# Performance work log

Hardware: AMD Instinct MI355X
Metric: run time of the kernel (lower is better)

## Reference

```python
import jax, jax.numpy as jnp
import numpy as np

SEQ, BATCH, DIM = 2048, 32, 1024


def setup_inputs() -> dict:
    key = jax.random.key(0)
    k1, k2, k3, k4, k5 = jax.random.split(key, 5)
    scale = 1.0 / np.sqrt(DIM)
    return {
        "decoder_hidden": jax.random.normal(k1, (BATCH, 1, DIM), dtype=jnp.float32),
        "encoder_out": jax.random.normal(k2, (SEQ, BATCH, DIM), dtype=jnp.float32),
        "W_enc": jax.random.normal(k3, (DIM, DIM), dtype=jnp.float32) * scale,
        "W_dec": jax.random.normal(k4, (DIM, DIM), dtype=jnp.float32) * scale,
        "V_att": jax.random.normal(k5, (1, DIM), dtype=jnp.float32) * scale,
    }


def reference(decoder_hidden, encoder_out, W_enc, W_dec, V_att):
    # encoder_out: (seq, batch, dim); decoder_hidden: (batch, 1, dim)
    # torch Linear: y = x @ W.T with W of shape (out, in)
    keys = jnp.einsum('sbd,ed->bse', encoder_out, W_enc)      # (batch, seq, dim)
    query = decoder_hidden @ W_dec.T                           # (batch, 1, dim)
    scores = jnp.tanh(keys + query)                            # (batch, seq, dim)
    logits = jnp.einsum('bsd,d->bs', scores, V_att[0])         # (batch, seq)
    alpha = jax.nn.softmax(logits, axis=1)[..., None]          # (batch, seq, 1)
    # context = alpha^T @ encoder_out_permuted -> (batch, 1, dim)
    context = jnp.einsum('bs,sbd->bd', alpha[..., 0], encoder_out)[:, None, :]
    return context, jnp.transpose(alpha, (2, 0, 1))            # (1, batch, seq)
```

## Files before the change

### kernel.cpp

```cpp
#include <hip/hip_runtime.h>
#include <hip/hip_bf16.h>
#include <math.h>

#define SEQ   2048
#define BATCH 32
#define DIM   1024
#define MROWS (SEQ*BATCH)
#define NT2   4
#define NCH   16
#define NKT   16

typedef __attribute__((ext_vector_type(8))) short short8;
typedef __attribute__((ext_vector_type(8))) unsigned short u16x8;
typedef __attribute__((ext_vector_type(4))) float f32x4;

__device__ __forceinline__ unsigned short f2bf(float f) {
  unsigned u = __builtin_bit_cast(unsigned, f);
  u += 0x7FFFu + ((u >> 16) & 1u);
  return (unsigned short)(u >> 16);
}

__device__ __forceinline__ void gl16(const unsigned short* g, unsigned short* l) {
  __builtin_amdgcn_global_load_lds(
      (const __attribute__((address_space(1))) unsigned int*)g,
      (__attribute__((address_space(3))) unsigned int*)l, 16, 0, 0);
}

__global__ __launch_bounds__(256) void conv_bf16_k(const float* __restrict__ src,
                                                   unsigned short* __restrict__ dst) {
  size_t i = ((size_t)blockIdx.x * 256 + threadIdx.x) * 8;
  f32x4 a = __builtin_nontemporal_load(reinterpret_cast<const f32x4*>(src + i));
  f32x4 b = __builtin_nontemporal_load(reinterpret_cast<const f32x4*>(src + i + 4));
  u16x8 o;
  o[0] = f2bf(a[0]); o[1] = f2bf(a[1]); o[2] = f2bf(a[2]); o[3] = f2bf(a[3]);
  o[4] = f2bf(b[0]); o[5] = f2bf(b[1]); o[6] = f2bf(b[2]); o[7] = f2bf(b[3]);
  *reinterpret_cast<u16x8*>(dst + i) = o;
}

__global__ __launch_bounds__(256) void qpart_k(const float* __restrict__ dh,
                                               const float* __restrict__ Wd,
                                               float* __restrict__ qpart) {
  const int bx = blockIdx.x;
  const int eb = bx & 3;
  const int dc = bx >> 2;
  __shared__ float ldh[BATCH][128];
  const int tid = threadIdx.x;
#pragma unroll
  for (int i = 0; i < 4; ++i) {
    int idx = tid + i * 256;
    int bb = idx >> 5, d4 = idx & 31;
    float4 v = *reinterpret_cast<const float4*>(&dh[(size_t)bb * DIM + dc * 128 + d4 * 4]);
    *reinterpret_cast<float4*>(&ldh[bb][d4 * 4]) = v;
  }
  __syncthreads();
  const int e = eb * 256 + tid;
  float acc[BATCH];
#pragma unroll
  for (int b = 0; b < BATCH; ++b) acc[b] = 0.f;
  for (int d4 = 0; d4 < 32; ++d4) {
    float4 w = *reinterpret_cast<const float4*>(&Wd[(size_t)e * DIM + dc * 128 + d4 * 4]);
#pragma unroll
    for (int b = 0; b < BATCH; ++b) {
      float4 h = *reinterpret_cast<const float4*>(&ldh[b][d4 * 4]);
      acc[b] += w.x * h.x + w.y * h.y + w.z * h.z + w.w * h.w;
    }
  }
#pragma unroll
  for (int b = 0; b < BATCH; ++b)
    qpart[((size_t)dc * BATCH + b) * DIM + e] = acc[b];
}

__global__ __launch_bounds__(256) void qred_k(const float* __restrict__ qpart,
                                              float* __restrict__ q) {
  int i = blockIdx.x * 256 + threadIdx.x;
  float s = 0.f;
#pragma unroll
  for (int dc = 0; dc < 8; ++dc) s += qpart[(size_t)dc * 32768 + i];
  q[i] = s;
}

#define BARR  __builtin_amdgcn_s_barrier()
#define VMC(n) asm volatile("s_waitcnt vmcnt(" #n ")" ::: "memory")

#define STAGE_A(t, h) do {                                                        \
    const unsigned short* gb_ = Abase + (size_t)(t) * 64;                         \
    char* lb_ = arena + (((t) & 1) * 65536) + (h) * 16384;                        \
    gl16(gb_ + (size_t)(gA0 + (h) * 64) * 1024 + cSt * 8,                         \
         (unsigned short*)lb_ + w * 512);                                         \
    gl16(gb_ + (size_t)(gA0 + 128 + (h) * 64) * 1024 + cSt * 8,                   \
         (unsigned short*)(lb_ + 8192) + w * 512);                                \
  } while (0)

#define STAGE_B(t, h) do {                                                        \
    const unsigned short* gb_ = Bbase + (size_t)(t) * 64;                         \
    char* lb_ = arena + (((t) & 1) * 65536) + 32768 + (h) * 16384;                \
    gl16(gb_ + (size_t)(gB0 + (h) * 32) * 1024 + cSt * 8,                         \
         (unsigned short*)lb_ + w * 512);                                         \
    gl16(gb_ + (size_t)(gB0 + 128 + (h) * 32) * 1024 + cSt * 8,                   \
         (unsigned short*)(lb_ + 8192) + w * 512);                                \
  } while (0)

#define LOAD_A(d, MH) do {                                                        \
    const char* bA_ = arena + (d) * 65536 + (MH) * 16384;                         \
    _Pragma("unroll") for (int i_ = 0; i_ < 4; ++i_)                              \
    _Pragma("unroll") for (int ks_ = 0; ks_ < 2; ++ks_) {                         \
      int lrow_ = wr * 64 + i_ * 16 + fr;                                         \
      int lc_ = (ks_ * 4 + kq) ^ (fr & 7);                                        \
      a[i_][ks_] = *(const short8*)(bA_ + lrow_ * 128 + lc_ * 16);                \
    } } while (0)

#define LOAD_B(d, NH) do {                                                        \
    const char* bB_ = arena + (d) * 65536 + 32768 + (NH) * 16384;                 \
    _Pragma("unroll") for (int j_ = 0; j_ < 2; ++j_)                              \
    _Pragma("unroll") for (int ks_ = 0; ks_ < 2; ++ks_) {                         \
      int lrow_ = wc * 32 + j_ * 16 + fr;                                         \
      int lc_ = (ks_ * 4 + kq) ^ (fr & 7);                                        \
      b[NH][j_][ks_] = *(const short8*)(bB_ + lrow_ * 128 + lc_ * 16);            \
    } } while (0)

#define DO_QUAD(MH, NH) do {                                                      \
    __builtin_amdgcn_s_setprio(1);                                                \
    _Pragma("unroll") for (int i_ = 0; i_ < 4; ++i_)                              \
    _Pragma("unroll") for (int j_ = 0; j_ < 2; ++j_)                              \
    _Pragma("unroll") for (int ks_ = 0; ks_ < 2; ++ks_)                           \
      acc[(MH) * 4 + i_][(NH) * 2 + j_] =                                         \
          __builtin_amdgcn_mfma_f32_16x16x32_bf16(                                \
              a[i_][ks_], b[NH][j_][ks_], acc[(MH) * 4 + i_][(NH) * 2 + j_],      \
              0, 0, 0);                                                           \
    __builtin_amdgcn_s_setprio(0);                                                \
  } while (0)

__global__ __launch_bounds__(512, 2) void gemm8p(const unsigned short* __restrict__ A,
                                                 const unsigned short* __restrict__ B,
                                                 const float* __restrict__ q,
                                                 const float* __restrict__ V,
                                                 float* __restrict__ lpart) {
  __shared__ __align__(16) char arena[131072];

  const int bid = blockIdx.x;
  const int wg = (bid & 7) * 128 + (bid >> 3);
  const int mt = wg >> 2, nt = wg & 3;
  const int row0 = mt * 256, col0 = nt * 256;
  const int tid = threadIdx.x;
  const int lane = tid & 63, w = tid >> 6;
  const int wr = w >> 2, wc = w & 3;
  const int fr = lane & 15, kq = lane >> 4;

  const int lr0 = tid >> 3;
  const int cSt = (tid & 7) ^ (lr0 & 7);
  const int gA0 = lr0;
  const int gB0 = (lr0 & 31) + (lr0 >> 5) * 64;

  const unsigned short* Abase = A + (size_t)row0 * DIM;
  const unsigned short* Bbase = B + (size_t)col0 * DIM;

  f32x4 acc[8][4];
#pragma unroll
  for (int i = 0; i < 8; ++i)
#pragma unroll
    for (int j = 0; j < 4; ++j) acc[i][j] = (f32x4)(0.f);

  short8 a[4][2];
  short8 b[2][2][2];

  STAGE_A(0, 0); STAGE_B(0, 0); STAGE_A(0, 1); STAGE_B(0, 1);
  STAGE_A(1, 0); STAGE_B(1, 0);
  VMC(0);
  BARR;

#pragma unroll 1
  for (int t2 = 0; t2 < NKT; t2 += 2) {
    const bool last = (t2 == NKT - 2);
    LOAD_A(0, 0); LOAD_B(0, 0);
    STAGE_A(t2 + 1, 1);
    BARR; DO_QUAD(0, 0); BARR;
    LOAD_B(0, 1);
    STAGE_B(t2 + 1, 1);
    BARR; DO_QUAD(0, 1); BARR;
    LOAD_A(0, 1);
    if (!last) STAGE_A(t2 + 2, 0);
    BARR; DO_QUAD(1, 0); BARR;
    if (!last) { STAGE_B(t2 + 2, 0); VMC(4); } else { VMC(0); }
    BARR; DO_QUAD(1, 1); BARR;
    LOAD_A(1, 0); LOAD_B(1, 0);
    if (!last) STAGE_A(t2 + 2, 1);
    BARR; DO_QUAD(0, 0); BARR;
    LOAD_B(1, 1);
    if (!last) STAGE_B(t2 + 2, 1);
    BARR; DO_QUAD(0, 1); BARR;
    LOAD_A(1, 1);
    if (!last) STAGE_A(t2 + 3, 0);
    BARR; DO_QUAD(1, 0); BARR;
    if (!last) { STAGE_B(t2 + 3, 0); VMC(4); }
    BARR; DO_QUAD(1, 1); BARR;
  }

  __syncthreads();
  float* qld = (float*)arena;
  float* vld = (float*)(arena + 33280);
  float* red = (float*)(arena + 34304);
#pragma unroll
  for (int i = 0; i < 4; ++i) {
    int id = i * 512 + tid;
    int bb = id >> 6, e4 = id & 63;
    float4 v = *(const float4*)&q[(size_t)bb * DIM + col0 + e4 * 4];
    *(float4*)&qld[bb * 260 + e4 * 4] = v;
  }
  if (tid < 64) *(float4*)&vld[tid * 4] = *(const float4*)&V[col0 + tid * 4];
  __syncthreads();

#pragma unroll
  for (int mf = 0; mf < 8; ++mf) {
#pragma unroll
    for (int reg = 0; reg < 4; ++reg) {
      const int m_loc = wr * 128 + mf * 16 + kq * 4 + reg;
      const int bb = m_loc & 31;
      float val = 0.f;
#pragma unroll
      for (int nf = 0; nf < 4; ++nf) {
        const int el = wc * 64 + nf * 16 + fr;
        float x = acc[mf][nf][reg] + qld[bb * 260 + el];
        float g = __expf(2.f * x);
        float tnh = 1.f - 2.f * __builtin_amdgcn_rcpf(g + 1.f);
        val += tnh * vld[el];
      }
      val += __shfl_xor(val, 1); val += __shfl_xor(val, 2);
      val += __shfl_xor(val, 4); val += __shfl_xor(val, 8);
      if (fr == 0) red[wc * 256 + m_loc] = val;
    }
  }
  __syncthreads();
  if (tid < 256) {
    float s = red[tid] + red[256 + tid] + red[512 + tid] + red[768 + tid];
    lpart[(size_t)(row0 + tid) * NT2 + nt] = s;
  }
}

__global__ __launch_bounds__(256) void softmax_k(const float* __restrict__ lpart,
                                                 float* __restrict__ alpha) {
  const int b = blockIdx.x;
  __shared__ float lv[SEQ];
  __shared__ float sred[4];
  const int tid = threadIdx.x;
  float mx = -1e30f;
  for (int s = tid; s < SEQ; s += 256) {
    const float* p = &lpart[(size_t)(s * BATCH + b) * NT2];
    float v = p[0] + p[1] + p[2] + p[3];
    lv[s] = v;
    mx = fmaxf(mx, v);
  }
#pragma unroll
  for (int off = 32; off >= 1; off >>= 1) mx = fmaxf(mx, __shfl_xor(mx, off));
  if ((tid & 63) == 0) sred[tid >> 6] = mx;
  __syncthreads();
  mx = fmaxf(fmaxf(sred[0], sred[1]), fmaxf(sred[2], sred[3]));
  __syncthreads();
  float sm = 0.f;
  for (int s = tid; s < SEQ; s += 256) {
    float e = expf(lv[s] - mx);
    lv[s] = e;
    sm += e;
  }
#pragma unroll
  for (int off = 32; off >= 1; off >>= 1) sm += __shfl_xor(sm, off);
  if ((tid & 63) == 0) sred[tid >> 6] = sm;
  __syncthreads();
  const float inv = 1.f / (sred[0] + sred[1] + sred[2] + sred[3]);
  for (int s = tid; s < SEQ; s += 256)
    alpha[(size_t)b * SEQ + s] = lv[s] * inv;
}

__global__ __launch_bounds__(256) void ctx_part_k(const unsigned short* __restrict__ encbf,
                                                  const float* __restrict__ alpha,
                                                  float* __restrict__ cpart) {
  const int blk = blockIdx.x;
  const int b = blk & 31;
  const int ch = blk >> 5;
  const int tid = threadIdx.x;
  const int g = tid >> 7;
  const int d0 = (tid & 127) * 8;
  const int s0 = ch * (SEQ / NCH);
  float acc8[8];
#pragma unroll
  for (int k = 0; k < 8; ++k) acc8[k] = 0.f;
#pragma unroll 4
  for (int i = 0; i < SEQ / NCH; i += 2) {
    const int s = s0 + i + g;
    const float a = alpha[(size_t)b * SEQ + s];
    u16x8 v = *reinterpret_cast<const u16x8*>(&encbf[((size_t)s * BATCH + b) * DIM + d0]);
#pragma unroll
    for (int k = 0; k < 8; ++k) {
      float f = __builtin_bit_cast(float, (unsigned)v[k] << 16);
      acc8[k] += a * f;
    }
  }
  size_t o = ((size_t)(ch * 2 + g) * BATCH + b) * DIM + d0;
  float4 lo = {acc8[0], acc8[1], acc8[2], acc8[3]};
  float4 hi = {acc8[4], acc8[5], acc8[6], acc8[7]};
  *(float4*)&cpart[o] = lo;
  *(float4*)&cpart[o + 4] = hi;
}

__global__ __launch_bounds__(256) void ctxred_k(const float* __restrict__ cpart,
                                                float* __restrict__ out) {
  int i = blockIdx.x * 256 + threadIdx.x;
  float s = 0.f;
#pragma unroll
  for (int ch = 0; ch < 32; ++ch) s += cpart[(size_t)ch * 32768 + i];
  out[i] = s;
}

extern "C" void kernel_launch(void* const* d_in, const int* in_sizes, int n_in,
                              void* d_out, int out_size, void* d_ws, size_t ws_size,
                              hipStream_t stream) {
  const float* dh   = (const float*)d_in[0];
  const float* enc  = (const float*)d_in[1];
  const float* Wenc = (const float*)d_in[2];
  const float* Wdec = (const float*)d_in[3];
  const float* Vatt = (const float*)d_in[4];
  float* out = (float*)d_out;

  float* ws = (float*)d_ws;
  float* q      = ws;
  float* qpart  = ws + 32768;
  float* lpart  = ws + 294912;
  float* cpart  = ws + 557056;
  unsigned short* Wbf   = (unsigned short*)(ws + 1605632);
  unsigned short* encbf = (unsigned short*)(ws + 2129920);

  conv_bf16_k<<<dim3(512),   dim3(256), 0, stream>>>(Wenc, Wbf);
  qpart_k    <<<dim3(32),    dim3(256), 0, stream>>>(dh, Wdec, qpart);
  qred_k     <<<dim3(128),   dim3(256), 0, stream>>>(qpart, q);
  conv_bf16_k<<<dim3(32768), dim3(256), 0, stream>>>(enc, encbf);
  gemm8p     <<<dim3(1024),  dim3(512), 0, stream>>>(encbf, Wbf, q, Vatt, lpart);
  softmax_k  <<<dim3(BATCH),     dim3(256), 0, stream>>>(lpart, out + 32768);
  ctx_part_k <<<dim3(BATCH*NCH), dim3(256), 0, stream>>>(encbf, out + 32768, cpart);
  ctxred_k   <<<dim3(128),       dim3(256), 0, stream>>>(cpart, out);
}
```

Measured before the change: 274.1 us.

## Merge GEMM main-loop phases from eight to four per double-tile

Restructures the software-pipelined GEMM loop so each phase loads both B halves into separate register sets and issues two MFMA quads between one barrier pair. Global-to-LDS staging of A and B halves is grouped per phase. This halves the number of barriers and scheduling phases per iteration, cutting synchronization overhead. In exchange it uses more registers at once, changes the vmcnt wait points (the prologue now waits with VMC(4)), and risks correctness if data is read before its staging has arrived.

```diff
diff --git a/kernel.cpp b/kernel.cpp
--- a/kernel.cpp
+++ b/kernel.cpp
@@ -109,23 +109,23 @@
       a[i_][ks_] = *(const short8*)(bA_ + lrow_ * 128 + lc_ * 16);                \
     } } while (0)
 
-#define LOAD_B(d, NH) do {                                                        \
+#define LOAD_B(SET, d, NH) do {                                                   \
     const char* bB_ = arena + (d) * 65536 + 32768 + (NH) * 16384;                 \
     _Pragma("unroll") for (int j_ = 0; j_ < 2; ++j_)                              \
     _Pragma("unroll") for (int ks_ = 0; ks_ < 2; ++ks_) {                         \
       int lrow_ = wc * 32 + j_ * 16 + fr;                                         \
       int lc_ = (ks_ * 4 + kq) ^ (fr & 7);                                        \
-      b[NH][j_][ks_] = *(const short8*)(bB_ + lrow_ * 128 + lc_ * 16);            \
+      SET[j_][ks_] = *(const short8*)(bB_ + lrow_ * 128 + lc_ * 16);              \
     } } while (0)
 
-#define DO_QUAD(MH, NH) do {                                                      \
+#define QUAD(BSET, MH, NH) do {                                                   \
     __builtin_amdgcn_s_setprio(1);                                                \
     _Pragma("unroll") for (int i_ = 0; i_ < 4; ++i_)                              \
     _Pragma("unroll") for (int j_ = 0; j_ < 2; ++j_)                              \
     _Pragma("unroll") for (int ks_ = 0; ks_ < 2; ++ks_)                           \
       acc[(MH) * 4 + i_][(NH) * 2 + j_] =                                         \
           __builtin_amdgcn_mfma_f32_16x16x32_bf16(                                \
-              a[i_][ks_], b[NH][j_][ks_], acc[(MH) * 4 + i_][(NH) * 2 + j_],      \
+              a[i_][ks_], BSET[j_][ks_], acc[(MH) * 4 + i_][(NH) * 2 + j_],       \
               0, 0, 0);                                                           \
     __builtin_amdgcn_s_setprio(0);                                                \
   } while (0)
@@ -161,38 +161,28 @@
     for (int j = 0; j < 4; ++j) acc[i][j] = (f32x4)(0.f);
 
   short8 a[4][2];
-  short8 b[2][2][2];
+  short8 b0[2][2], b1[2][2];
 
   STAGE_A(0, 0); STAGE_B(0, 0); STAGE_A(0, 1); STAGE_B(0, 1);
   STAGE_A(1, 0); STAGE_B(1, 0);
-  VMC(0);
+  VMC(4);
   BARR;
 
 #pragma unroll 1
   for (int t2 = 0; t2 < NKT; t2 += 2) {
     const bool last = (t2 == NKT - 2);
-    LOAD_A(0, 0); LOAD_B(0, 0);
-    STAGE_A(t2 + 1, 1);
-    BARR; DO_QUAD(0, 0); BARR;
-    LOAD_B(0, 1);
-    STAGE_B(t2 + 1, 1);
-    BARR; DO_QUAD(0, 1); BARR;
+    LOAD_A(0, 0); LOAD_B(b0, 0, 0); LOAD_B(b1, 0, 1);
+    STAGE_A(t2 + 1, 1); STAGE_B(t2 + 1, 1);
+    BARR; QUAD(b0, 0, 0); QUAD(b1, 0, 1); BARR;
     LOAD_A(0, 1);
-    if (!last) STAGE_A(t2 + 2, 0);
-    BARR; DO_QUAD(1, 0); BARR;
-    if (!last) { STAGE_B(t2 + 2, 0); VMC(4); } else { VMC(0); }
-    BARR; DO_QUAD(1, 1); BARR;
-    LOAD_A(1, 0); LOAD_B(1, 0);
-    if (!last) STAGE_A(t2 + 2, 1);
-    BARR; DO_QUAD(0, 0); BARR;
-    LOAD_B(1, 1);
-    if (!last) STAGE_B(t2 + 2, 1);
-    BARR; DO_QUAD(0, 1); BARR;
+    if (!last) { STAGE_A(t2 + 2, 0); STAGE_B(t2 + 2, 0); VMC(4); } else { VMC(0); }
+    BARR; QUAD(b0, 1, 0); QUAD(b1, 1, 1); BARR;
+    LOAD_A(1, 0); LOAD_B(b0, 1, 0); LOAD_B(b1, 1, 1);
+    if (!last) { STAGE_A(t2 + 2, 1); STAGE_B(t2 + 2, 1); }
+    BARR; QUAD(b0, 0, 0); QUAD(b1, 0, 1); BARR;
     LOAD_A(1, 1);
-    if (!last) STAGE_A(t2 + 3, 0);
-    BARR; DO_QUAD(1, 0); BARR;
-    if (!last) { STAGE_B(t2 + 3, 0); VMC(4); }
-    BARR; DO_QUAD(1, 1); BARR;
+    if (!last) { STAGE_A(t2 + 3, 0); STAGE_B(t2 + 3, 0); VMC(4); }
+    BARR; QUAD(b0, 1, 0); QUAD(b1, 1, 1); BARR;
   }
 
   __syncthreads();
```

Result: no change. 274.2 us (+0.1%).
